# Kernel tuning notes

Measured on AMD Instinct MI355X. Metric: run time of the kernel, lower is better.

## Reference

```python
import jax, jax.numpy as jnp
import numpy as np

B, H, W, C = 2, 128, 128, 128
K = 3            # window_size
NB = K * K       # neighbor_count = 9
RP = 8           # relative_position_dim
HID = 128        # edge hidden = max(256//2, 128)
EIN = 3 * C + RP # edge_input_dim = 392
CLIP = 3.0
GEPS = 1e-06     # gate_eps
LNE = 1e-05      # LayerNorm eps


def _ln(x, g, b):
    m = x.mean(-1, keepdims=True)
    v = ((x - m) ** 2).mean(-1, keepdims=True)
    return (x - m) * jax.lax.rsqrt(v + LNE) * g + b


def setup_inputs() -> dict:
    key = jax.random.key(0)
    ks = jax.random.split(key, 12)
    f32 = jnp.float32
    inp = {
        'tokens': jax.random.normal(ks[0], (B, H, W, C), dtype=f32),
        'ln1_g': jnp.ones((C,), f32), 'ln1_b': jnp.zeros((C,), f32),
        'ln2_g': jnp.ones((C,), f32), 'ln2_b': jnp.zeros((C,), f32),
        'rel_pos': 0.02 * jax.random.normal(ks[1], (NB, RP), dtype=f32),
        'dW1': 0.01 * jax.random.normal(ks[2], (EIN, HID), dtype=f32),
        'db1': jnp.zeros((HID,), f32),
        'dW2': 0.01 * jax.random.normal(ks[3], (HID, 1), dtype=f32),
        'db2': jnp.zeros((1,), f32),
        'rW1': 0.01 * jax.random.normal(ks[4], (EIN, HID), dtype=f32),
        'rb1': jnp.zeros((HID,), f32),
        'rW2': 0.01 * jax.random.normal(ks[5], (HID, 1), dtype=f32),
        'rb2': jnp.zeros((1,), f32),
        'vW': 0.01 * jax.random.normal(ks[6], (C, C), dtype=f32),
        'vb': jnp.zeros((C,), f32),
        'oW': 0.01 * jax.random.normal(ks[7], (C, C), dtype=f32),
        'ob': jnp.zeros((C,), f32),
        'eml_gamma': jnp.asarray(0.1, f32),
        'eml_lam': jnp.asarray(1.0, f32),
        'eml_bias': jnp.asarray(-0.3, f32),
    }
    return inp


def _edge_mlp(x, W1, b1, W2, b2):
    h = jax.nn.gelu(jnp.einsum('blnd,dh->blnh', x, W1) + b1, approximate=False)
    return jnp.einsum('blnh,ho->blno', h, W2) + b2


def _forward(tokens, ln1_g, ln1_b, ln2_g, ln2_b, rel_pos, dW1, db1, dW2, db2,
             rW1, rb1, rW2, rb2, vW, vb, oW, ob, eml_gamma, eml_lam, eml_bias,
             warmup_eta=1.0):
    Bh, Hh, Wh, Ch = tokens.shape
    L = Hh * Wh
    normalized = _ln(tokens, ln1_g, ln1_b)
    flat = normalized.reshape(Bh, L, Ch)
    # Unfold(kernel=3, padding=1): gather 9 shifted views, then replicate torch's
    # reshape of the (C, 9)-ordered channel axis into (9, C).
    pad = jnp.pad(normalized, ((0, 0), (1, 1), (1, 1), (0, 0)))
    shifts = [pad[:, i:i + Hh, j:j + Wh, :] for i in range(K) for j in range(K)]
    nbhd = jnp.stack(shifts, axis=-1)                       # [B,H,W,C,9]
    nbhd = nbhd.reshape(Bh, L, Ch * NB).reshape(Bh, L, NB, Ch)  # torch reshape semantics
    center = jnp.broadcast_to(flat[:, :, None, :], nbhd.shape)
    rel = jnp.broadcast_to(rel_pos[None, None], (Bh, L, NB, rel_pos.shape[-1]))
    edge_features = jnp.concatenate([center, nbhd, center - nbhd, rel], axis=-1)
    drive = _edge_mlp(edge_features, dW1, db1, dW2, db2)[..., 0]        # [B,L,9]
    resistance = _edge_mlp(edge_features, rW1, rb1, rW2, rb2)[..., 0]   # [B,L,9]
    # EML unit (Ohm's-law style gate): clamp(eta*gamma*drive/(lambda*softplus(R)+eps)+bias)
    energy = jnp.clip(
        warmup_eta * (eml_gamma * drive) / (eml_lam * jax.nn.softplus(resistance) + GEPS)
        + eml_bias, -CLIP, CLIP)
    gate = jax.nn.sigmoid(energy)                                        # [B,L,9]
    values = jnp.einsum('blnc,cd->blnd', nbhd, vW) + vb                  # [B,L,9,C]
    gate_mass = jnp.maximum(gate.sum(axis=2), GEPS)                      # [B,L]
    message = jnp.einsum('bln,blnc->blc', gate, values) / gate_mass[..., None]
    update = (jnp.einsum('blc,cd->bld', message, oW) + ob).reshape(Bh, Hh, Wh, Ch)
    output = _ln(tokens + update, ln2_g, ln2_b)  # dropout is identity at eval
    return output


def reference(tokens, ln1_g, ln1_b, ln2_g, ln2_b, rel_pos, dW1, db1, dW2, db2,
              rW1, rb1, rW2, rb2, vW, vb, oW, ob, eml_gamma, eml_lam, eml_bias):
    return _forward(tokens, ln1_g, ln1_b, ln2_g, ln2_b, rel_pos, dW1, db1, dW2, db2,
                    rW1, rb1, rW2, rb2, vW, vb, oW, ob, eml_gamma, eml_lam, eml_bias)
```

## Files before the change

### kernel.cpp

```cpp
#include <hip/hip_runtime.h>


#define USHORT unsigned short
#define AW 152

typedef __attribute__((ext_vector_type(8)))  __bf16 v8bf;
typedef __attribute__((ext_vector_type(8)))  USHORT v8u;
typedef __attribute__((ext_vector_type(16))) float  v16f;

__device__ __forceinline__ USHORT f2bf(float f) {
    unsigned v; __builtin_memcpy(&v, &f, 4);
    v += 0x7FFFu + ((v >> 16) & 1u);
    return (USHORT)(v >> 16);
}

template <int C>
__device__ __forceinline__ float dpps(float x) {
    return __int_as_float(
        __builtin_amdgcn_update_dpp(0, __float_as_int(x), C, 0xf, 0xf, true));
}
__device__ __forceinline__ float red32half(float x) {
    x += dpps<0x111>(x);
    x += dpps<0x112>(x);
    x += dpps<0x114>(x);
    x += dpps<0x118>(x);
    x += dpps<0x142>(x);
    return x;
}
__device__ __forceinline__ float red64(float x) {
    x = red32half(x);
    x += dpps<0x143>(x);
    return x;
}
__device__ __forceinline__ float bcast63(float x) {
    return __int_as_float(__builtin_amdgcn_readlane(__float_as_int(x), 63));
}

__global__ __launch_bounds__(256) void k_setup(
    const float* __restrict__ tok, const float* __restrict__ ln1g,
    const float* __restrict__ ln1b,
    const float* __restrict__ dW1, const float* __restrict__ db1,
    const float* __restrict__ rW1, const float* __restrict__ rb1,
    const float* __restrict__ rel, const float* __restrict__ dW2,
    const float* __restrict__ rW2, const float* __restrict__ vW,
    const float* __restrict__ vb,  const float* __restrict__ oW,
    USHORT* __restrict__ norm,
    USHORT* __restrict__ WnTg, USHORT* __restrict__ WcTg, USHORT* __restrict__ VTg,
    float* __restrict__ preg, float* __restrict__ vboWg, float* __restrict__ w2g)
{
    const int blk = blockIdx.x, t = threadIdx.x;
    if (blk >= 354) {
        const int p = (blk - 354) * 4 + (t >> 6);
        const int lane = t & 63;
        const float2 x = ((const float2*)(tok + (size_t)p * 128))[lane];
        float s = x.x + x.y;
        for (int m = 1; m < 64; m <<= 1) s += __shfl_xor(s, m);
        const float mean = s * (1.f / 128.f);
        const float d0 = x.x - mean, d1 = x.y - mean;
        float q = d0 * d0 + d1 * d1;
        for (int m = 1; m < 64; m <<= 1) q += __shfl_xor(q, m);
        const float rstd = rsqrtf(q * (1.f / 128.f) + 1e-5f);
        const float2 gg = ((const float2*)ln1g)[lane], bb = ((const float2*)ln1b)[lane];
        ((unsigned*)norm)[(size_t)p * 64 + lane] =
            (unsigned)f2bf(d0 * rstd * gg.x + bb.x) |
            ((unsigned)f2bf(d1 * rstd * gg.y + bb.y) << 16);
        return;
    }
    if (blk < 72) {
        int idx = blk * 256 + t;
        int n = ((idx >> 4) * 7282) >> 16;
        int k = idx - n * 144;
        int r = k >> 4, tt = k & 15, c2 = r + 9 * tt;
        float acc = 0.f;
        if (c2 < 128)
            for (int j = 0; j < 128; ++j) acc += vW[c2 * 128 + j] * oW[j * 128 + n];
        VTg[idx] = f2bf(acc);
    } else if (blk < 216) {
        int idx = (blk - 72) * 256 + t;
        int n = ((idx >> 4) * 7282) >> 16;
        int k = idx - n * 144;
        int r = k >> 4, tt = k & 15, c2 = r + 9 * tt;
        int col = n & 127;
        const float* W = (n < 128) ? dW1 : rW1;
        float val = 0.f;
        if (c2 < 128) val = W[(128 + c2) * 128 + col] - W[(256 + c2) * 128 + col];
        WnTg[idx] = f2bf(val);
    } else if (blk < 344) {
        int idx = (blk - 216) * 256 + t;
        int n = idx >> 7, c = idx & 127, col = n & 127;
        const float* W = (n < 128) ? dW1 : rW1;
        WcTg[idx] = f2bf(W[c * 128 + col] + W[(256 + c) * 128 + col]);
    } else if (blk < 353) {
        int n2 = blk - 344; int h = t;
        float acc;
        if (h < 128) {
            acc = db1[h];
            for (int r = 0; r < 8; ++r) acc += rel[n2 * 8 + r] * dW1[(384 + r) * 128 + h];
        } else {
            int hh = h - 128;
            acc = rb1[hh];
            for (int r = 0; r < 8; ++r) acc += rel[n2 * 8 + r] * rW1[(384 + r) * 128 + hh];
        }
        preg[n2 * 256 + h] = acc;
    } else {
        if (t < 128) {
            float acc = 0.f;
            for (int j = 0; j < 128; ++j) acc += vb[j] * oW[j * 128 + t];
            vboWg[t] = acc;
            w2g[t] = dW2[t];
            w2g[128 + t] = rW2[t];
        }
    }
}

__device__ __forceinline__ void gather_load(
    uint2 (&pf)[9], const USHORT* __restrict__ nb,
    int n2, int y, int bI, int tid)
{
    const int x = tid >> 2, q = tid & 3;
    #pragma unroll
    for (int r = 0; r < 9; ++r) {
        int u = 2 * n2 + r;
        int n = (u >= 18) ? (u - 18) : ((u >= 9) ? (u - 9) : u);
        int v = n2 * 128 + r;
        int c0 = (v * 7282) >> 16;
        int dyq = (n * 22) >> 6;
        int dx = n - 3 * dyq - 1;
        int dy = dyq - 1;
        int sy = y + dy, sx = x + dx;
        bool ok = ((unsigned)sy < 128u) && ((unsigned)sx < 128u);
        int e0 = (c0 & ~1) + 4 * q;
        size_t gidx = ((size_t)((bI * 128 + (ok ? sy : 0)) * 128 + (ok ? sx : 0))) * 128 + e0;
        const unsigned* gp = (const unsigned*)nb + (gidx >> 1);
        unsigned dw0 = gp[0], dw1 = gp[1];
        pf[r].x = ok ? dw0 : 0u;
        pf[r].y = ok ? dw1 : 0u;
    }
}

__device__ __forceinline__ void gather_store(
    USHORT* __restrict__ Adst, const uint2 (&pf)[9], int n2, int tid)
{
    const int x = tid >> 2, q = tid & 3;
    #pragma unroll
    for (int r = 0; r < 9; ++r) {
        int v = n2 * 128 + r;
        int c0 = (v * 7282) >> 16;
        unsigned dw0 = pf[r].x, dw1 = pf[r].y;
        unsigned nxt = (unsigned)__shfl_down((int)dw0, 1);
        unsigned o0, o1;
        if (c0 & 1) { o0 = (dw0 >> 16) | (dw1 << 16); o1 = (dw1 >> 16) | (nxt << 16); }
        else        { o0 = dw0;                       o1 = dw1; }
        *(uint2*)(Adst + x * AW + 16 * r + 4 * q) = make_uint2(o0, o1);
    }
}

__global__ __launch_bounds__(512, 2) void k_edge(
    const float* __restrict__ tok, const float* __restrict__ ln2g,
    const float* __restrict__ ln2b, const USHORT* __restrict__ nb,
    const USHORT* __restrict__ WnTg, const USHORT* __restrict__ WcTg,
    const USHORT* __restrict__ VTg, const float* __restrict__ preg,
    const float* __restrict__ vboWg, const float* __restrict__ w2g,
    const float* __restrict__ db2p, const float* __restrict__ rb2p,
    const float* __restrict__ gmp, const float* __restrict__ lmp,
    const float* __restrict__ bip, const float* __restrict__ obp,
    float* __restrict__ out)
{
    extern __shared__ char smem[];
    USHORT* Wsh  = (USHORT*)smem;
    USHORT* Ash0 = (USHORT*)(smem + 77824);
    USHORT* Ash1 = (USHORT*)(smem + 116736);
    float*  w2L  = (float*)(smem + 155648);
    float*  dP   = (float*)(smem + 156672);
    float*  rP   = (float*)(smem + 157696);
    float*  gateL= (float*)(smem + 158720);
    float*  sgL  = (float*)(smem + 159232);
    float*  updF = (float*)smem;

    const int tid = threadIdx.x;
    const int lane = tid & 63, wave = tid >> 6, hi = lane >> 5, l31 = lane & 31;
    const int mw = wave & 1, nw = wave >> 1;
    const int blk = blockIdx.x;
    const int bI = blk >> 7;
    const int y = ((blk & 7) << 4) | ((blk >> 3) & 15);
    const int p0 = (bI * 128 + y) * 128;

    for (int i = tid; i < 4096; i += 512) {
        int n = i >> 4, kv = i & 15;
        *(v8u*)(Wsh + n * AW + kv * 8) = *(const v8u*)(WcTg + n * 128 + kv * 8);
    }
    for (int i = tid; i < 2048; i += 512) {
        int x = i >> 4, kv = i & 15;
        *(v8u*)(Ash0 + x * AW + kv * 8) = *(const v8u*)(nb + (size_t)(p0 + x) * 128 + kv * 8);
    }
    if (tid < 256) w2L[tid] = w2g[tid];
    if (tid < 128) sgL[tid] = 0.f;
    __syncthreads();

    v16f cp[2][2];
    #pragma unroll
    for (int a = 0; a < 2; ++a)
        for (int b = 0; b < 2; ++b)
            for (int e = 0; e < 16; ++e) cp[a][b][e] = 0.f;
    #pragma unroll
    for (int ks = 0; ks < 8; ++ks) {
        v8bf af0 = *(const v8bf*)(Ash0 + (mw * 64 + l31) * AW + ks * 16 + hi * 8);
        v8bf af1 = *(const v8bf*)(Ash0 + (mw * 64 + 32 + l31) * AW + ks * 16 + hi * 8);
        v8bf bf0 = *(const v8bf*)(Wsh + (nw * 64 + l31) * AW + ks * 16 + hi * 8);
        v8bf bf1 = *(const v8bf*)(Wsh + (nw * 64 + 32 + l31) * AW + ks * 16 + hi * 8);
        cp[0][0] = __builtin_amdgcn_mfma_f32_32x32x16_bf16(af0, bf0, cp[0][0], 0, 0, 0);
        cp[0][1] = __builtin_amdgcn_mfma_f32_32x32x16_bf16(af0, bf1, cp[0][1], 0, 0, 0);
        cp[1][0] = __builtin_amdgcn_mfma_f32_32x32x16_bf16(af1, bf0, cp[1][0], 0, 0, 0);
        cp[1][1] = __builtin_amdgcn_mfma_f32_32x32x16_bf16(af1, bf1, cp[1][1], 0, 0, 0);
    }
    __syncthreads();

    for (int i = tid; i < 4608; i += 512) {
        int n = (i * 3641) >> 16;
        int kv = i - n * 18;
        *(v8u*)(Wsh + n * AW + kv * 8) = *(const v8u*)(WnTg + n * 144 + kv * 8);
    }
    {
        uint2 pf0[9];
        gather_load(pf0, nb, 0, y, bI, tid);
        gather_store(Ash0, pf0, 0, tid);
    }

    const float gmv = gmp[0], lmv = lmp[0], biv = bip[0];
    const float db2v = db2p[0], rb2v = rb2p[0];
    const float wv0 = w2L[nw * 64 + l31];
    const float wv1 = w2L[nw * 64 + 32 + l31];

    float G[36];
    #pragma unroll
    for (int j = 0; j < 36; ++j) G[j] = 0.f;
    const int grow = tid >> 2, gq = tid & 3;

    float* sumBase = ((nw < 2) ? dP : rP) + (nw & 1) * 128;

    __syncthreads();

    for (int n2 = 0; n2 < 9; ++n2) {
        USHORT* Acur = (n2 & 1) ? Ash1 : Ash0;
        USHORT* Anxt = (n2 & 1) ? Ash0 : Ash1;
        const float pv0 = preg[n2 * 256 + nw * 64 + l31];
        const float pv1 = preg[n2 * 256 + nw * 64 + 32 + l31];

        uint2 pf[9];
        if (n2 < 8) gather_load(pf, nb, n2 + 1, y, bI, tid);

        v16f acc[2][2];
        #pragma unroll
        for (int a = 0; a < 2; ++a)
            for (int b = 0; b < 2; ++b) acc[a][b] = cp[a][b];
        #pragma unroll
        for (int ks = 0; ks < 9; ++ks) {
            v8bf af0 = *(const v8bf*)(Acur + (mw * 64 + l31) * AW + ks * 16 + hi * 8);
            v8bf af1 = *(const v8bf*)(Acur + (mw * 64 + 32 + l31) * AW + ks * 16 + hi * 8);
            v8bf bf0 = *(const v8bf*)(Wsh + (nw * 64 + l31) * AW + ks * 16 + hi * 8);
            v8bf bf1 = *(const v8bf*)(Wsh + (nw * 64 + 32 + l31) * AW + ks * 16 + hi * 8);
            acc[0][0] = __builtin_amdgcn_mfma_f32_32x32x16_bf16(af0, bf0, acc[0][0], 0, 0, 0);
            acc[0][1] = __builtin_amdgcn_mfma_f32_32x32x16_bf16(af0, bf1, acc[0][1], 0, 0, 0);
            acc[1][0] = __builtin_amdgcn_mfma_f32_32x32x16_bf16(af1, bf0, acc[1][0], 0, 0, 0);
            acc[1][1] = __builtin_amdgcn_mfma_f32_32x32x16_bf16(af1, bf1, acc[1][1], 0, 0, 0);
        }
        #pragma unroll
        for (int mt = 0; mt < 2; ++mt) {
            float part[16];
            #pragma unroll
            for (int rr = 0; rr < 16; ++rr) {
                float h0 = acc[mt][0][rr] + pv0;
                float h1 = acc[mt][1][rr] + pv1;
                float s0 = __builtin_amdgcn_rcpf(1.f + __expf(-1.702f * h0));
                float s1 = __builtin_amdgcn_rcpf(1.f + __expf(-1.702f * h1));
                part[rr] = h0 * s0 * wv0 + h1 * s1 * wv1;
            }
            #pragma unroll
            for (int rr = 0; rr < 16; ++rr) part[rr] = red32half(part[rr]);
            if (l31 == 31) {
                float* t0 = sumBase + ((mw * 2 + mt) * 2 + hi) * 16;
                *(float4*)(t0 +  0) = make_float4(part[0],  part[1],  part[2],  part[3]);
                *(float4*)(t0 +  4) = make_float4(part[4],  part[5],  part[6],  part[7]);
                *(float4*)(t0 +  8) = make_float4(part[8],  part[9],  part[10], part[11]);
                *(float4*)(t0 + 12) = make_float4(part[12], part[13], part[14], part[15]);
            }
        }
        __syncthreads();
        if (n2 < 8) gather_store(Anxt, pf, n2 + 1, tid);
        if (tid < 128) {
            int w32 = tid & 31;
            int slot = (((tid >> 6) * 2 + ((tid >> 5) & 1)) * 2 + ((w32 >> 2) & 1)) * 16
                       + ((w32 & 3) | (((w32 >> 3) & 3) << 2));
            float d = dP[slot] + dP[128 + slot] + db2v;
            float rr = rP[slot] + rP[128 + slot] + rb2v;
            float sp = fmaxf(rr, 0.f) + log1pf(__expf(-fabsf(rr)));
            float e = gmv * d / (lmv * sp + 1e-6f) + biv;
            e = fminf(fmaxf(e, -3.f), 3.f);
            float gt = 1.f / (1.f + __expf(-e));
            gateL[tid] = gt; sgL[tid] += gt;
        }
        __syncthreads();
        {
            const float g = gateL[grow];
            const USHORT* Ar = Acur + grow * AW + gq * 36;
            #pragma unroll
            for (int j = 0; j < 9; ++j) {
                uint2 wv = *(const uint2*)(Ar + 4 * j);
                float v0 = __int_as_float((int)(wv.x << 16));
                float v1 = __int_as_float((int)(wv.x & 0xFFFF0000u));
                float v2 = __int_as_float((int)(wv.y << 16));
                float v3 = __int_as_float((int)(wv.y & 0xFFFF0000u));
                G[4 * j + 0] += g * v0;
                G[4 * j + 1] += g * v1;
                G[4 * j + 2] += g * v2;
                G[4 * j + 3] += g * v3;
            }
        }
    }

    __syncthreads();

    {
        USHORT* dst = Ash0 + grow * AW + gq * 36;
        #pragma unroll
        for (int j = 0; j < 9; ++j) {
            unsigned lo = (unsigned)f2bf(G[4 * j + 0]) | ((unsigned)f2bf(G[4 * j + 1]) << 16);
            unsigned hi2 = (unsigned)f2bf(G[4 * j + 2]) | ((unsigned)f2bf(G[4 * j + 3]) << 16);
            *(uint2*)(dst + 4 * j) = make_uint2(lo, hi2);
        }
    }
    for (int i = tid; i < 2304; i += 512) {
        int n = (i * 3641) >> 16;
        int kv = i - n * 18;
        *(v8u*)(Ash1 + n * AW + kv * 8) = *(const v8u*)(VTg + n * 144 + kv * 8);
    }
    if (tid < 128) {
        float s = sgL[tid];
        float m = fmaxf(s, 1e-6f);
        dP[tid] = 1.f / m;
        rP[tid] = s / m;
    }
    __syncthreads();

    v16f P[2];
    #pragma unroll
    for (int a = 0; a < 2; ++a)
        for (int e = 0; e < 16; ++e) P[a][e] = 0.f;
    #pragma unroll
    for (int ks = 0; ks < 9; ++ks) {
        v8bf af0 = *(const v8bf*)(Ash0 + (mw * 64 + l31) * AW + ks * 16 + hi * 8);
        v8bf af1 = *(const v8bf*)(Ash0 + (mw * 64 + 32 + l31) * AW + ks * 16 + hi * 8);
        v8bf vf  = *(const v8bf*)(Ash1 + (nw * 32 + l31) * AW + ks * 16 + hi * 8);
        P[0] = __builtin_amdgcn_mfma_f32_32x32x16_bf16(af0, vf, P[0], 0, 0, 0);
        P[1] = __builtin_amdgcn_mfma_f32_32x32x16_bf16(af1, vf, P[1], 0, 0, 0);
    }

    {
        const int colc = nw * 32 + l31;
        const float vbw = vboWg[colc], obv = obp[colc];
        #pragma unroll
        for (int mt = 0; mt < 2; ++mt) {
            const int base = mw * 64 + mt * 32 + 4 * hi;
            const float4* iq = (const float4*)&dP[base];
            const float4* sq = (const float4*)&rP[base];
            float4 ia = iq[0], ib = iq[2], ic = iq[4], id = iq[6];
            float4 sa = sq[0], sb = sq[2], sc = sq[4], sd = sq[6];
            float iv[16] = {ia.x, ia.y, ia.z, ia.w, ib.x, ib.y, ib.z, ib.w,
                            ic.x, ic.y, ic.z, ic.w, id.x, id.y, id.z, id.w};
            float sv[16] = {sa.x, sa.y, sa.z, sa.w, sb.x, sb.y, sb.z, sb.w,
                            sc.x, sc.y, sc.z, sc.w, sd.x, sd.y, sd.z, sd.w};
            #pragma unroll
            for (int rr = 0; rr < 16; ++rr) {
                int row = base + (rr & 3) + 8 * (rr >> 2);
                updF[row * 128 + colc] = P[mt][rr] * iv[rr] + vbw * sv[rr] + obv;
            }
        }
    }
    __syncthreads();

    const float g20 = ln2g[lane], g21 = ln2g[lane + 64];
    const float b20 = ln2b[lane], b21 = ln2b[lane + 64];
    for (int q2 = 0; q2 < 16; ++q2) {
        int p = wave * 16 + q2;
        size_t gp = (size_t)(p0 + p) * 128;
        float x0 = tok[gp + lane]      + updF[p * 128 + lane];
        float x1 = tok[gp + lane + 64] + updF[p * 128 + lane + 64];
        float mean = bcast63(red64(x0 + x1)) * (1.f / 128.f);
        float d0 = x0 - mean, d1 = x1 - mean;
        float rstd = rsqrtf(bcast63(red64(d0 * d0 + d1 * d1)) * (1.f / 128.f) + 1e-5f);
        out[gp + lane]      = d0 * rstd * g20 + b20;
        out[gp + lane + 64] = d1 * rstd * g21 + b21;
    }
}

extern "C" void kernel_launch(void* const* d_in, const int* in_sizes, int n_in,
                              void* d_out, int out_size, void* d_ws, size_t ws_size,
                              hipStream_t stream) {
    const float* tok  = (const float*)d_in[0];
    const float* ln1g = (const float*)d_in[1];
    const float* ln1b = (const float*)d_in[2];
    const float* ln2g = (const float*)d_in[3];
    const float* ln2b = (const float*)d_in[4];
    const float* rel  = (const float*)d_in[5];
    const float* dW1  = (const float*)d_in[6];
    const float* db1  = (const float*)d_in[7];
    const float* dW2  = (const float*)d_in[8];
    const float* db2  = (const float*)d_in[9];
    const float* rW1  = (const float*)d_in[10];
    const float* rb1  = (const float*)d_in[11];
    const float* rW2  = (const float*)d_in[12];
    const float* rb2  = (const float*)d_in[13];
    const float* vW   = (const float*)d_in[14];
    const float* vb   = (const float*)d_in[15];
    const float* oW   = (const float*)d_in[16];
    const float* ob   = (const float*)d_in[17];
    const float* gm   = (const float*)d_in[18];
    const float* lm   = (const float*)d_in[19];
    const float* bi   = (const float*)d_in[20];
    float* out = (float*)d_out;

    char* w = (char*)d_ws;
    USHORT* norm = (USHORT*)w; w += 8388608;
    USHORT* WnTg = (USHORT*)w; w += 73728;
    USHORT* WcTg = (USHORT*)w; w += 65536;
    USHORT* VTg  = (USHORT*)w; w += 36864;
    float*  preg = (float*)w;  w += 9216;
    float*  vboWg= (float*)w;  w += 512;
    float*  w2g  = (float*)w;  w += 1024;

    hipFuncSetAttribute((const void*)k_edge,
                        hipFuncAttributeMaxDynamicSharedMemorySize, 159744);

    hipLaunchKernelGGL(k_setup, dim3(8546), dim3(256), 0, stream,
                       tok, ln1g, ln1b, dW1, db1, rW1, rb1, rel, dW2, rW2,
                       vW, vb, oW, norm, WnTg, WcTg, VTg, preg, vboWg, w2g);
    hipLaunchKernelGGL(k_edge, dim3(256), dim3(512), 159744, stream,
                       tok, ln2g, ln2b, norm, WnTg, WcTg, VTg, preg, vboWg, w2g,
                       db2, rb2, gm, lm, bi, ob, out);
}
```

Before: 185.8 us.

## Double edge-kernel waves to 1024 threads and single-buffer the neighbor tile

The edge kernel moves from 512 to 1024 threads per block, so each wave owns a 32-row M tile instead of 64, halving per-wave accumulators and MFMA work. The gather now moves one dword per thread instead of two. The A tile drops double buffering: the next neighbor is written into the same LDS buffer after a barrier, and the gated accumulation reads the shifted values kept in registers rather than reading LDS. This frees the second buffer, so the V-weight load is hoisted to the start of the kernel. The aim is more resident waves for latency hiding and less LDS traffic, at the cost of less overlap between the gather and the MFMAs and more barrier participants.

After: 199.4 us. 7.4% more time.

```diff
diff --git a/kernel.cpp b/kernel.cpp
--- a/kernel.cpp
+++ b/kernel.cpp
@@ -113,11 +113,11 @@
     }
 }
 
-__device__ __forceinline__ void gather_load(
-    uint2 (&pf)[9], const USHORT* __restrict__ nb,
+__device__ __forceinline__ void gather_load9(
+    unsigned (&raw)[9], const USHORT* __restrict__ nb,
     int n2, int y, int bI, int tid)
 {
-    const int x = tid >> 2, q = tid & 3;
+    const int x = tid >> 3, q = tid & 7;
     #pragma unroll
     for (int r = 0; r < 9; ++r) {
         int u = 2 * n2 + r;
@@ -129,33 +129,30 @@
         int dy = dyq - 1;
         int sy = y + dy, sx = x + dx;
         bool ok = ((unsigned)sy < 128u) && ((unsigned)sx < 128u);
-        int e0 = (c0 & ~1) + 4 * q;
+        int e0 = (c0 & ~1) + 2 * q;
         size_t gidx = ((size_t)((bI * 128 + (ok ? sy : 0)) * 128 + (ok ? sx : 0))) * 128 + e0;
-        const unsigned* gp = (const unsigned*)nb + (gidx >> 1);
-        unsigned dw0 = gp[0], dw1 = gp[1];
-        pf[r].x = ok ? dw0 : 0u;
-        pf[r].y = ok ? dw1 : 0u;
-    }
-}
-
-__device__ __forceinline__ void gather_store(
-    USHORT* __restrict__ Adst, const uint2 (&pf)[9], int n2, int tid)
+        unsigned dw = *((const unsigned*)nb + (gidx >> 1));
+        raw[r] = ok ? dw : 0u;
+    }
+}
+
+__device__ __forceinline__ void shift_store9(
+    USHORT* __restrict__ Adst, const unsigned (&raw)[9], unsigned (&o)[9],
+    int n2, int tid)
 {
-    const int x = tid >> 2, q = tid & 3;
+    const int x = tid >> 3, q = tid & 7;
     #pragma unroll
     for (int r = 0; r < 9; ++r) {
         int v = n2 * 128 + r;
         int c0 = (v * 7282) >> 16;
-        unsigned dw0 = pf[r].x, dw1 = pf[r].y;
-        unsigned nxt = (unsigned)__shfl_down((int)dw0, 1);
-        unsigned o0, o1;
-        if (c0 & 1) { o0 = (dw0 >> 16) | (dw1 << 16); o1 = (dw1 >> 16) | (nxt << 16); }
-        else        { o0 = dw0;                       o1 = dw1; }
-        *(uint2*)(Adst + x * AW + 16 * r + 4 * q) = make_uint2(o0, o1);
-    }
-}
-
-__global__ __launch_bounds__(512, 2) void k_edge(
+        unsigned nxt = (unsigned)__shfl_down((int)raw[r], 1);
+        unsigned oo = (c0 & 1) ? ((raw[r] >> 16) | (nxt << 16)) : raw[r];
+        o[r] = oo;
+        *(unsigned*)(Adst + x * AW + 16 * r + 2 * q) = oo;
+    }
+}
+
+__global__ __launch_bounds__(1024, 3) void k_edge(
     const float* __restrict__ tok, const float* __restrict__ ln2g,
     const float* __restrict__ ln2b, const USHORT* __restrict__ nb,
     const USHORT* __restrict__ WnTg, const USHORT* __restrict__ WcTg,
@@ -179,51 +176,53 @@
 
     const int tid = threadIdx.x;
     const int lane = tid & 63, wave = tid >> 6, hi = lane >> 5, l31 = lane & 31;
-    const int mw = wave & 1, nw = wave >> 1;
+    const int mw = wave & 3, nw = wave >> 2;
     const int blk = blockIdx.x;
     const int bI = blk >> 7;
     const int y = ((blk & 7) << 4) | ((blk >> 3) & 15);
     const int p0 = (bI * 128 + y) * 128;
 
-    for (int i = tid; i < 4096; i += 512) {
+    for (int i = tid; i < 4096; i += 1024) {
         int n = i >> 4, kv = i & 15;
         *(v8u*)(Wsh + n * AW + kv * 8) = *(const v8u*)(WcTg + n * 128 + kv * 8);
     }
-    for (int i = tid; i < 2048; i += 512) {
+    for (int i = tid; i < 2048; i += 1024) {
         int x = i >> 4, kv = i & 15;
         *(v8u*)(Ash0 + x * AW + kv * 8) = *(const v8u*)(nb + (size_t)(p0 + x) * 128 + kv * 8);
     }
+    for (int i = tid; i < 2304; i += 1024) {
+        int n = (i * 3641) >> 16;
+        int kv = i - n * 18;
+        *(v8u*)(Ash1 + n * AW + kv * 8) = *(const v8u*)(VTg + n * 144 + kv * 8);
+    }
     if (tid < 256) w2L[tid] = w2g[tid];
     if (tid < 128) sgL[tid] = 0.f;
     __syncthreads();
 
-    v16f cp[2][2];
-    #pragma unroll
-    for (int a = 0; a < 2; ++a)
-        for (int b = 0; b < 2; ++b)
-            for (int e = 0; e < 16; ++e) cp[a][b][e] = 0.f;
+    v16f cp[2];
+    #pragma unroll
+    for (int b = 0; b < 2; ++b)
+        for (int e = 0; e < 16; ++e) cp[b][e] = 0.f;
     #pragma unroll
     for (int ks = 0; ks < 8; ++ks) {
-        v8bf af0 = *(const v8bf*)(Ash0 + (mw * 64 + l31) * AW + ks * 16 + hi * 8);
-        v8bf af1 = *(const v8bf*)(Ash0 + (mw * 64 + 32 + l31) * AW + ks * 16 + hi * 8);
+        v8bf af0 = *(const v8bf*)(Ash0 + (mw * 32 + l31) * AW + ks * 16 + hi * 8);
         v8bf bf0 = *(const v8bf*)(Wsh + (nw * 64 + l31) * AW + ks * 16 + hi * 8);
         v8bf bf1 = *(const v8bf*)(Wsh + (nw * 64 + 32 + l31) * AW + ks * 16 + hi * 8);
-        cp[0][0] = __builtin_amdgcn_mfma_f32_32x32x16_bf16(af0, bf0, cp[0][0], 0, 0, 0);
-        cp[0][1] = __builtin_amdgcn_mfma_f32_32x32x16_bf16(af0, bf1, cp[0][1], 0, 0, 0);
-        cp[1][0] = __builtin_amdgcn_mfma_f32_32x32x16_bf16(af1, bf0, cp[1][0], 0, 0, 0);
-        cp[1][1] = __builtin_amdgcn_mfma_f32_32x32x16_bf16(af1, bf1, cp[1][1], 0, 0, 0);
-    }
-    __syncthreads();
-
-    for (int i = tid; i < 4608; i += 512) {
+        cp[0] = __builtin_amdgcn_mfma_f32_32x32x16_bf16(af0, bf0, cp[0], 0, 0, 0);
+        cp[1] = __builtin_amdgcn_mfma_f32_32x32x16_bf16(af0, bf1, cp[1], 0, 0, 0);
+    }
+    __syncthreads();
+
+    for (int i = tid; i < 4608; i += 1024) {
         int n = (i * 3641) >> 16;
         int kv = i - n * 18;
         *(v8u*)(Wsh + n * AW + kv * 8) = *(const v8u*)(WnTg + n * 144 + kv * 8);
     }
+    unsigned pfc[9];
     {
-        uint2 pf0[9];
-        gather_load(pf0, nb, 0, y, bI, tid);
-        gather_store(Ash0, pf0, 0, tid);
+        unsigned raw0[9];
+        gather_load9(raw0, nb, 0, y, bI, tid);
+        shift_store9(Ash0, raw0, pfc, 0, tid);
     }
 
     const float gmv = gmp[0], lmv = lmp[0], biv = bip[0];
@@ -231,46 +230,39 @@
     const float wv0 = w2L[nw * 64 + l31];
     const float wv1 = w2L[nw * 64 + 32 + l31];
 
-    float G[36];
-    #pragma unroll
-    for (int j = 0; j < 36; ++j) G[j] = 0.f;
-    const int grow = tid >> 2, gq = tid & 3;
+    float G[18];
+    #pragma unroll
+    for (int j = 0; j < 18; ++j) G[j] = 0.f;
+    const int grow = tid >> 3;
 
     float* sumBase = ((nw < 2) ? dP : rP) + (nw & 1) * 128;
 
     __syncthreads();
 
     for (int n2 = 0; n2 < 9; ++n2) {
-        USHORT* Acur = (n2 & 1) ? Ash1 : Ash0;
-        USHORT* Anxt = (n2 & 1) ? Ash0 : Ash1;
         const float pv0 = preg[n2 * 256 + nw * 64 + l31];
         const float pv1 = preg[n2 * 256 + nw * 64 + 32 + l31];
 
-        uint2 pf[9];
-        if (n2 < 8) gather_load(pf, nb, n2 + 1, y, bI, tid);
-
-        v16f acc[2][2];
+        unsigned raw[9];
+        if (n2 < 8) gather_load9(raw, nb, n2 + 1, y, bI, tid);
+
+        v16f acc[2];
         #pragma unroll
-        for (int a = 0; a < 2; ++a)
-            for (int b = 0; b < 2; ++b) acc[a][b] = cp[a][b];
+        for (int b = 0; b < 2; ++b) acc[b] = cp[b];
         #pragma unroll
         for (int ks = 0; ks < 9; ++ks) {
-            v8bf af0 = *(const v8bf*)(Acur + (mw * 64 + l31) * AW + ks * 16 + hi * 8);
-            v8bf af1 = *(const v8bf*)(Acur + (mw * 64 + 32 + l31) * AW + ks * 16 + hi * 8);
+            v8bf af0 = *(const v8bf*)(Ash0 + (mw * 32 + l31) * AW + ks * 16 + hi * 8);
             v8bf bf0 = *(const v8bf*)(Wsh + (nw * 64 + l31) * AW + ks * 16 + hi * 8);
             v8bf bf1 = *(const v8bf*)(Wsh + (nw * 64 + 32 + l31) * AW + ks * 16 + hi * 8);
-            acc[0][0] = __builtin_amdgcn_mfma_f32_32x32x16_bf16(af0, bf0, acc[0][0], 0, 0, 0);
-            acc[0][1] = __builtin_amdgcn_mfma_f32_32x32x16_bf16(af0, bf1, acc[0][1], 0, 0, 0);
-            acc[1][0] = __builtin_amdgcn_mfma_f32_32x32x16_bf16(af1, bf0, acc[1][0], 0, 0, 0);
-            acc[1][1] = __builtin_amdgcn_mfma_f32_32x32x16_bf16(af1, bf1, acc[1][1], 0, 0, 0);
-        }
-        #pragma unroll
-        for (int mt = 0; mt < 2; ++mt) {
+            acc[0] = __builtin_amdgcn_mfma_f32_32x32x16_bf16(af0, bf0, acc[0], 0, 0, 0);
+            acc[1] = __builtin_amdgcn_mfma_f32_32x32x16_bf16(af0, bf1, acc[1], 0, 0, 0);
+        }
+        {
             float part[16];
             #pragma unroll
             for (int rr = 0; rr < 16; ++rr) {
-                float h0 = acc[mt][0][rr] + pv0;
-                float h1 = acc[mt][1][rr] + pv1;
+                float h0 = acc[0][rr] + pv0;
+                float h1 = acc[1][rr] + pv1;
                 float s0 = __builtin_amdgcn_rcpf(1.f + __expf(-1.702f * h0));
                 float s1 = __builtin_amdgcn_rcpf(1.f + __expf(-1.702f * h1));
                 part[rr] = h0 * s0 * wv0 + h1 * s1 * wv1;
@@ -278,7 +270,7 @@
             #pragma unroll
             for (int rr = 0; rr < 16; ++rr) part[rr] = red32half(part[rr]);
             if (l31 == 31) {
-                float* t0 = sumBase + ((mw * 2 + mt) * 2 + hi) * 16;
+                float* t0 = sumBase + (mw * 2 + hi) * 16;
                 *(float4*)(t0 +  0) = make_float4(part[0],  part[1],  part[2],  part[3]);
                 *(float4*)(t0 +  4) = make_float4(part[4],  part[5],  part[6],  part[7]);
                 *(float4*)(t0 +  8) = make_float4(part[8],  part[9],  part[10], part[11]);
@@ -286,10 +278,11 @@
             }
         }
         __syncthreads();
-        if (n2 < 8) gather_store(Anxt, pf, n2 + 1, tid);
+        unsigned pfn[9];
+        if (n2 < 8) shift_store9(Ash0, raw, pfn, n2 + 1, tid);
         if (tid < 128) {
             int w32 = tid & 31;
-            int slot = (((tid >> 6) * 2 + ((tid >> 5) & 1)) * 2 + ((w32 >> 2) & 1)) * 16
+            int slot = (tid >> 5) * 32 + ((w32 >> 2) & 1) * 16
                        + ((w32 & 3) | (((w32 >> 3) & 3) << 2));
             float d = dP[slot] + dP[128 + slot] + db2v;
             float rr = rP[slot] + rP[128 + slot] + rb2v;
@@ -302,37 +295,31 @@
         __syncthreads();
         {
             const float g = gateL[grow];
-            const USHORT* Ar = Acur + grow * AW + gq * 36;
             #pragma unroll
-            for (int j = 0; j < 9; ++j) {
-                uint2 wv = *(const uint2*)(Ar + 4 * j);
-                float v0 = __int_as_float((int)(wv.x << 16));
-                float v1 = __int_as_float((int)(wv.x & 0xFFFF0000u));
-                float v2 = __int_as_float((int)(wv.y << 16));
-                float v3 = __int_as_float((int)(wv.y & 0xFFFF0000u));
-                G[4 * j + 0] += g * v0;
-                G[4 * j + 1] += g * v1;
-                G[4 * j + 2] += g * v2;
-                G[4 * j + 3] += g * v3;
+            for (int r = 0; r < 9; ++r) {
+                unsigned oo = pfc[r];
+                float v0 = __int_as_float((int)(oo << 16));
+                float v1 = __int_as_float((int)(oo & 0xFFFF0000u));
+                G[2 * r]     += g * v0;
+                G[2 * r + 1] += g * v1;
             }
         }
+        if (n2 < 8) {
+            #pragma unroll
+            for (int r = 0; r < 9; ++r) pfc[r] = pfn[r];
+        }
     }
 
     __syncthreads();
 
     {
-        USHORT* dst = Ash0 + grow * AW + gq * 36;
+        const int q = tid & 7;
+        USHORT* dst = Ash0 + grow * AW + 2 * q;
         #pragma unroll
-        for (int j = 0; j < 9; ++j) {
-            unsigned lo = (unsigned)f2bf(G[4 * j + 0]) | ((unsigned)f2bf(G[4 * j + 1]) << 16);
-            unsigned hi2 = (unsigned)f2bf(G[4 * j + 2]) | ((unsigned)f2bf(G[4 * j + 3]) << 16);
-            *(uint2*)(dst + 4 * j) = make_uint2(lo, hi2);
-        }
-    }
-    for (int i = tid; i < 2304; i += 512) {
-        int n = (i * 3641) >> 16;
-        int kv = i - n * 18;
-        *(v8u*)(Ash1 + n * AW + kv * 8) = *(const v8u*)(VTg + n * 144 + kv * 8);
+        for (int r = 0; r < 9; ++r) {
+            unsigned pk = (unsigned)f2bf(G[2 * r]) | ((unsigned)f2bf(G[2 * r + 1]) << 16);
+            *(unsigned*)(dst + 16 * r) = pk;
+        }
     }
     if (tid < 128) {
         float s = sgL[tid];
@@ -342,46 +329,40 @@
     }
     __syncthreads();
 
-    v16f P[2];
-    #pragma unroll
-    for (int a = 0; a < 2; ++a)
-        for (int e = 0; e < 16; ++e) P[a][e] = 0.f;
+    v16f P;
+    #pragma unroll
+    for (int e = 0; e < 16; ++e) P[e] = 0.f;
     #pragma unroll
     for (int ks = 0; ks < 9; ++ks) {
-        v8bf af0 = *(const v8bf*)(Ash0 + (mw * 64 + l31) * AW + ks * 16 + hi * 8);
-        v8bf af1 = *(const v8bf*)(Ash0 + (mw * 64 + 32 + l31) * AW + ks * 16 + hi * 8);
+        v8bf af0 = *(const v8bf*)(Ash0 + (mw * 32 + l31) * AW + ks * 16 + hi * 8);
         v8bf vf  = *(const v8bf*)(Ash1 + (nw * 32 + l31) * AW + ks * 16 + hi * 8);
-        P[0] = __builtin_amdgcn_mfma_f32_32x32x16_bf16(af0, vf, P[0], 0, 0, 0);
-        P[1] = __builtin_amdgcn_mfma_f32_32x32x16_bf16(af1, vf, P[1], 0, 0, 0);
+        P = __builtin_amdgcn_mfma_f32_32x32x16_bf16(af0, vf, P, 0, 0, 0);
     }
 
     {
         const int colc = nw * 32 + l31;
         const float vbw = vboWg[colc], obv = obp[colc];
+        const int base = mw * 32 + 4 * hi;
+        const float4* iq = (const float4*)&dP[base];
+        const float4* sq = (const float4*)&rP[base];
+        float4 ia = iq[0], ib = iq[2], ic = iq[4], id = iq[6];
+        float4 sa = sq[0], sb = sq[2], sc = sq[4], sd = sq[6];
+        float iv[16] = {ia.x, ia.y, ia.z, ia.w, ib.x, ib.y, ib.z, ib.w,
+                        ic.x, ic.y, ic.z, ic.w, id.x, id.y, id.z, id.w};
+        float sv[16] = {sa.x, sa.y, sa.z, sa.w, sb.x, sb.y, sb.z, sb.w,
+                        sc.x, sc.y, sc.z, sc.w, sd.x, sd.y, sd.z, sd.w};
         #pragma unroll
-        for (int mt = 0; mt < 2; ++mt) {
-            const int base = mw * 64 + mt * 32 + 4 * hi;
-            const float4* iq = (const float4*)&dP[base];
-            const float4* sq = (const float4*)&rP[base];
-            float4 ia = iq[0], ib = iq[2], ic = iq[4], id = iq[6];
-            float4 sa = sq[0], sb = sq[2], sc = sq[4], sd = sq[6];
-            float iv[16] = {ia.x, ia.y, ia.z, ia.w, ib.x, ib.y, ib.z, ib.w,
-                            ic.x, ic.y, ic.z, ic.w, id.x, id.y, id.z, id.w};
-            float sv[16] = {sa.x, sa.y, sa.z, sa.w, sb.x, sb.y, sb.z, sb.w,
-                            sc.x, sc.y, sc.z, sc.w, sd.x, sd.y, sd.z, sd.w};
-            #pragma unroll
-            for (int rr = 0; rr < 16; ++rr) {
-                int row = base + (rr & 3) + 8 * (rr >> 2);
-                updF[row * 128 + colc] = P[mt][rr] * iv[rr] + vbw * sv[rr] + obv;
-            }
+        for (int rr = 0; rr < 16; ++rr) {
+            int row = base + (rr & 3) + 8 * (rr >> 2);
+            updF[row * 128 + colc] = P[rr] * iv[rr] + vbw * sv[rr] + obv;
         }
     }
     __syncthreads();
 
     const float g20 = ln2g[lane], g21 = ln2g[lane + 64];
     const float b20 = ln2b[lane], b21 = ln2b[lane + 64];
-    for (int q2 = 0; q2 < 16; ++q2) {
-        int p = wave * 16 + q2;
+    for (int q2 = 0; q2 < 8; ++q2) {
+        int p = wave * 8 + q2;
         size_t gp = (size_t)(p0 + p) * 128;
         float x0 = tok[gp + lane]      + updF[p * 128 + lane];
         float x1 = tok[gp + lane + 64] + updF[p * 128 + lane + 64];
@@ -434,7 +415,7 @@
     hipLaunchKernelGGL(k_setup, dim3(8546), dim3(256), 0, stream,
                        tok, ln1g, ln1b, dW1, db1, rW1, rb1, rel, dW2, rW2,
                        vW, vb, oW, norm, WnTg, WcTg, VTg, preg, vboWg, w2g);
-    hipLaunchKernelGGL(k_edge, dim3(256), dim3(512), 159744, stream,
+    hipLaunchKernelGGL(k_edge, dim3(256), dim3(1024), 159744, stream,
                        tok, ln2g, ln2b, norm, WnTg, WcTg, VTg, preg, vboWg, w2g,
                        db2, rb2, gm, lm, bi, ob, out);
 }
```

## Remove per-neighbor barrier by double-buffering partial sums and keeping gathered tiles in registers

Applied to the files above, without the earlier changes.

The per-neighbor edge-score partial sums are now double-buffered in shared memory by parity. This lets the second __syncthreads in each of the 9 iterations go away. Every thread computes its own gate redundantly instead of 128 threads writing it to shared memory, and accumulates the gated neighborhood from the shifted gather registers it already holds instead of re-reading the A tile from LDS. The final normalization reciprocal moves into the epilogue. This adds register pressure (a second 9-entry uint2 buffer, redundant transcendental math on all threads) and enlarges shared memory slightly, which could hurt occupancy at 2 blocks per CU.

New measurement: 187.7 us. About the same (+1.0%).

```diff
diff --git a/kernel.cpp b/kernel.cpp
--- a/kernel.cpp
+++ b/kernel.cpp
@@ -139,7 +139,7 @@
 }
 
 __device__ __forceinline__ void gather_store(
-    USHORT* __restrict__ Adst, const uint2 (&pf)[9], int n2, int tid)
+    USHORT* __restrict__ Adst, uint2 (&pf)[9], int n2, int tid)
 {
     const int x = tid >> 2, q = tid & 3;
     #pragma unroll
@@ -151,6 +151,7 @@
         unsigned o0, o1;
         if (c0 & 1) { o0 = (dw0 >> 16) | (dw1 << 16); o1 = (dw1 >> 16) | (nxt << 16); }
         else        { o0 = dw0;                       o1 = dw1; }
+        pf[r].x = o0; pf[r].y = o1;
         *(uint2*)(Adst + x * AW + 16 * r + 4 * q) = make_uint2(o0, o1);
     }
 }
@@ -172,9 +173,8 @@
     USHORT* Ash1 = (USHORT*)(smem + 116736);
     float*  w2L  = (float*)(smem + 155648);
     float*  dP   = (float*)(smem + 156672);
-    float*  rP   = (float*)(smem + 157696);
-    float*  gateL= (float*)(smem + 158720);
-    float*  sgL  = (float*)(smem + 159232);
+    float*  rP   = (float*)(smem + 158720);
+    float*  sgL  = (float*)(smem + 160768);
     float*  updF = (float*)smem;
 
     const int tid = threadIdx.x;
@@ -194,7 +194,6 @@
         *(v8u*)(Ash0 + x * AW + kv * 8) = *(const v8u*)(nb + (size_t)(p0 + x) * 128 + kv * 8);
     }
     if (tid < 256) w2L[tid] = w2g[tid];
-    if (tid < 128) sgL[tid] = 0.f;
     __syncthreads();
 
     v16f cp[2][2];
@@ -220,11 +219,9 @@
         int kv = i - n * 18;
         *(v8u*)(Wsh + n * AW + kv * 8) = *(const v8u*)(WnTg + n * 144 + kv * 8);
     }
-    {
-        uint2 pf0[9];
-        gather_load(pf0, nb, 0, y, bI, tid);
-        gather_store(Ash0, pf0, 0, tid);
-    }
+    uint2 pfc[9];
+    gather_load(pfc, nb, 0, y, bI, tid);
+    gather_store(Ash0, pfc, 0, tid);
 
     const float gmv = gmp[0], lmv = lmp[0], biv = bip[0];
     const float db2v = db2p[0], rb2v = rb2p[0];
@@ -234,20 +231,26 @@
     float G[36];
     #pragma unroll
     for (int j = 0; j < 36; ++j) G[j] = 0.f;
+    float sg = 0.f;
     const int grow = tid >> 2, gq = tid & 3;
 
-    float* sumBase = ((nw < 2) ? dP : rP) + (nw & 1) * 128;
+    const int w32g = grow & 31;
+    const int gslot = (((grow >> 6) * 2 + ((grow >> 5) & 1)) * 2 + ((w32g >> 2) & 1)) * 16
+                      + ((w32g & 3) | (((w32g >> 3) & 3) << 2));
+
+    float* sumHalf = ((nw < 2) ? dP : rP) + (nw & 1) * 128;
 
     __syncthreads();
 
     for (int n2 = 0; n2 < 9; ++n2) {
-        USHORT* Acur = (n2 & 1) ? Ash1 : Ash0;
-        USHORT* Anxt = (n2 & 1) ? Ash0 : Ash1;
+        const int par = n2 & 1;
+        USHORT* Acur = par ? Ash1 : Ash0;
+        USHORT* Anxt = par ? Ash0 : Ash1;
         const float pv0 = preg[n2 * 256 + nw * 64 + l31];
         const float pv1 = preg[n2 * 256 + nw * 64 + 32 + l31];
 
-        uint2 pf[9];
-        if (n2 < 8) gather_load(pf, nb, n2 + 1, y, bI, tid);
+        uint2 raw[9];
+        if (n2 < 8) gather_load(raw, nb, n2 + 1, y, bI, tid);
 
         v16f acc[2][2];
         #pragma unroll
@@ -278,55 +281,47 @@
             #pragma unroll
             for (int rr = 0; rr < 16; ++rr) part[rr] = red32half(part[rr]);
             if (l31 == 31) {
-                float* t0 = sumBase + ((mw * 2 + mt) * 2 + hi) * 16;
+                float* t0 = sumHalf + par * 256 + ((mw * 2 + mt) * 2 + hi) * 16;
                 *(float4*)(t0 +  0) = make_float4(part[0],  part[1],  part[2],  part[3]);
                 *(float4*)(t0 +  4) = make_float4(part[4],  part[5],  part[6],  part[7]);
                 *(float4*)(t0 +  8) = make_float4(part[8],  part[9],  part[10], part[11]);
                 *(float4*)(t0 + 12) = make_float4(part[12], part[13], part[14], part[15]);
             }
         }
+        if (n2 < 8) gather_store(Anxt, raw, n2 + 1, tid);
         __syncthreads();
-        if (n2 < 8) gather_store(Anxt, pf, n2 + 1, tid);
-        if (tid < 128) {
-            int w32 = tid & 31;
-            int slot = (((tid >> 6) * 2 + ((tid >> 5) & 1)) * 2 + ((w32 >> 2) & 1)) * 16
-                       + ((w32 & 3) | (((w32 >> 3) & 3) << 2));
-            float d = dP[slot] + dP[128 + slot] + db2v;
-            float rr = rP[slot] + rP[128 + slot] + rb2v;
-            float sp = fmaxf(rr, 0.f) + log1pf(__expf(-fabsf(rr)));
+
+        {
+            const int pb = par * 256;
+            float d  = dP[pb + gslot] + dP[pb + 128 + gslot] + db2v;
+            float rv = rP[pb + gslot] + rP[pb + 128 + gslot] + rb2v;
+            float sp = fmaxf(rv, 0.f) + log1pf(__expf(-fabsf(rv)));
             float e = gmv * d / (lmv * sp + 1e-6f) + biv;
             e = fminf(fmaxf(e, -3.f), 3.f);
             float gt = 1.f / (1.f + __expf(-e));
-            gateL[tid] = gt; sgL[tid] += gt;
-        }
-        __syncthreads();
-        {
-            const float g = gateL[grow];
-            const USHORT* Ar = Acur + grow * AW + gq * 36;
+            sg += gt;
             #pragma unroll
-            for (int j = 0; j < 9; ++j) {
-                uint2 wv = *(const uint2*)(Ar + 4 * j);
-                float v0 = __int_as_float((int)(wv.x << 16));
-                float v1 = __int_as_float((int)(wv.x & 0xFFFF0000u));
-                float v2 = __int_as_float((int)(wv.y << 16));
-                float v3 = __int_as_float((int)(wv.y & 0xFFFF0000u));
-                G[4 * j + 0] += g * v0;
-                G[4 * j + 1] += g * v1;
-                G[4 * j + 2] += g * v2;
-                G[4 * j + 3] += g * v3;
+            for (int r = 0; r < 9; ++r) {
+                unsigned o0 = pfc[r].x, o1 = pfc[r].y;
+                G[4 * r + 0] += gt * __int_as_float((int)(o0 << 16));
+                G[4 * r + 1] += gt * __int_as_float((int)(o0 & 0xFFFF0000u));
+                G[4 * r + 2] += gt * __int_as_float((int)(o1 << 16));
+                G[4 * r + 3] += gt * __int_as_float((int)(o1 & 0xFFFF0000u));
             }
         }
-    }
-
-    __syncthreads();
+        if (n2 < 8) {
+            #pragma unroll
+            for (int r = 0; r < 9; ++r) pfc[r] = raw[r];
+        }
+    }
 
     {
-        USHORT* dst = Ash0 + grow * AW + gq * 36;
+        USHORT* dst = Ash0 + grow * AW + 4 * gq;
         #pragma unroll
-        for (int j = 0; j < 9; ++j) {
-            unsigned lo = (unsigned)f2bf(G[4 * j + 0]) | ((unsigned)f2bf(G[4 * j + 1]) << 16);
-            unsigned hi2 = (unsigned)f2bf(G[4 * j + 2]) | ((unsigned)f2bf(G[4 * j + 3]) << 16);
-            *(uint2*)(dst + 4 * j) = make_uint2(lo, hi2);
+        for (int r = 0; r < 9; ++r) {
+            unsigned lo  = (unsigned)f2bf(G[4 * r + 0]) | ((unsigned)f2bf(G[4 * r + 1]) << 16);
+            unsigned hi2 = (unsigned)f2bf(G[4 * r + 2]) | ((unsigned)f2bf(G[4 * r + 3]) << 16);
+            *(uint2*)(dst + 16 * r) = make_uint2(lo, hi2);
         }
     }
     for (int i = tid; i < 2304; i += 512) {
@@ -334,12 +329,7 @@
         int kv = i - n * 18;
         *(v8u*)(Ash1 + n * AW + kv * 8) = *(const v8u*)(VTg + n * 144 + kv * 8);
     }
-    if (tid < 128) {
-        float s = sgL[tid];
-        float m = fmaxf(s, 1e-6f);
-        dP[tid] = 1.f / m;
-        rP[tid] = s / m;
-    }
+    if (gq == 0) sgL[grow] = sg;
     __syncthreads();
 
     v16f P[2];
@@ -361,18 +351,16 @@
         #pragma unroll
         for (int mt = 0; mt < 2; ++mt) {
             const int base = mw * 64 + mt * 32 + 4 * hi;
-            const float4* iq = (const float4*)&dP[base];
-            const float4* sq = (const float4*)&rP[base];
-            float4 ia = iq[0], ib = iq[2], ic = iq[4], id = iq[6];
+            const float4* sq = (const float4*)&sgL[base];
             float4 sa = sq[0], sb = sq[2], sc = sq[4], sd = sq[6];
-            float iv[16] = {ia.x, ia.y, ia.z, ia.w, ib.x, ib.y, ib.z, ib.w,
-                            ic.x, ic.y, ic.z, ic.w, id.x, id.y, id.z, id.w};
-            float sv[16] = {sa.x, sa.y, sa.z, sa.w, sb.x, sb.y, sb.z, sb.w,
-                            sc.x, sc.y, sc.z, sc.w, sd.x, sd.y, sd.z, sd.w};
+            float sv16[16] = {sa.x, sa.y, sa.z, sa.w, sb.x, sb.y, sb.z, sb.w,
+                              sc.x, sc.y, sc.z, sc.w, sd.x, sd.y, sd.z, sd.w};
             #pragma unroll
             for (int rr = 0; rr < 16; ++rr) {
                 int row = base + (rr & 3) + 8 * (rr >> 2);
-                updF[row * 128 + colc] = P[mt][rr] * iv[rr] + vbw * sv[rr] + obv;
+                float s = sv16[rr];
+                float iv = 1.f / fmaxf(s, 1e-6f);
+                updF[row * 128 + colc] = P[mt][rr] * iv + vbw * (s * iv) + obv;
             }
         }
     }
@@ -429,12 +417,12 @@
     float*  w2g  = (float*)w;  w += 1024;
 
     hipFuncSetAttribute((const void*)k_edge,
-                        hipFuncAttributeMaxDynamicSharedMemorySize, 159744);
+                        hipFuncAttributeMaxDynamicSharedMemorySize, 161280);
 
     hipLaunchKernelGGL(k_setup, dim3(8546), dim3(256), 0, stream,
                        tok, ln1g, ln1b, dW1, db1, rW1, rb1, rel, dW2, rW2,
                        vW, vb, oW, norm, WnTg, WcTg, VTg, preg, vboWg, w2g);
-    hipLaunchKernelGGL(k_edge, dim3(256), dim3(512), 159744, stream,
+    hipLaunchKernelGGL(k_edge, dim3(256), dim3(512), 161280, stream,
                        tok, ln2g, ln2b, norm, WnTg, WcTg, VTg, preg, vboWg, w2g,
                        db2, rb2, gm, lm, bi, ob, out);
 }
```
